# Optimization experiments

Measured on AMD Instinct MI355X. Metric: run time of the kernel, lower is better.

## Reference

```python
import jax, jax.numpy as jnp
import numpy as np

OUT_H, OUT_W = 512, 512


def setup_inputs() -> dict:
    key = jax.random.key(0)
    k1, k2 = jax.random.split(key)
    U = jax.random.normal(k1, (8, 512, 512, 16), dtype=jnp.float32)
    # coarse deformation field (x/y offsets in normalized [-1,1] coords)
    flow = jax.random.normal(k2, (8, 64, 64, 2), dtype=jnp.float32) * 0.1
    return {"U": U, "flow": flow}


def _grid_sample_bilinear(U, x, y):
    """Faithful port of _interpolate: x, y in [-1,1] normalized coords, shape [B,oh,ow].
    Note the original maps (x+1)*W/2 (not (W-1)/2) and computes weights from the
    CLIPPED corner coordinates — we replicate that exactly."""
    B, H, W, C = U.shape
    x = (x + 1.0) * (W / 2.0)
    y = (y + 1.0) * (H / 2.0)
    x0 = jnp.floor(x).astype(jnp.int32)
    x1 = x0 + 1
    y0 = jnp.floor(y).astype(jnp.int32)
    y1 = y0 + 1
    x0 = jnp.clip(x0, 0, W - 1)
    x1 = jnp.clip(x1, 0, W - 1)
    y0 = jnp.clip(y0, 0, H - 1)
    y1 = jnp.clip(y1, 0, H - 1)
    b = jnp.arange(B, dtype=jnp.int32)[:, None, None]  # broadcast over oh, ow
    Ia = U[b, y0, x0]  # [B,oh,ow,C]
    Ib = U[b, y1, x0]
    Ic = U[b, y0, x1]
    Id = U[b, y1, x1]
    x0f = x0.astype(jnp.float32); x1f = x1.astype(jnp.float32)
    y0f = y0.astype(jnp.float32); y1f = y1.astype(jnp.float32)
    wa = ((x1f - x) * (y1f - y))[..., None]
    wb = ((x1f - x) * (y - y0f))[..., None]
    wc = ((x - x0f) * (y1f - y))[..., None]
    wd = ((x - x0f) * (y - y0f))[..., None]
    return wa * Ia + wb * Ib + wc * Ic + wd * Id


def reference(U, flow):
    B, H, W, C = U.shape
    # bicubic upsample of the coarse deformation field to output resolution
    V = jax.image.resize(flow, (B, OUT_H, OUT_W, 2), method="cubic")  # [B,oh,ow,2]
    # identity sampling grid in [-1,1]
    xs = jnp.linspace(-1.0, 1.0, OUT_W, dtype=jnp.float32)
    ys = jnp.linspace(-1.0, 1.0, OUT_H, dtype=jnp.float32)
    Xg, Yg = jnp.meshgrid(xs, ys)  # [oh,ow]
    x_s = V[..., 0] + Xg  # [B,oh,ow]
    y_s = V[..., 1] + Yg
    return _grid_sample_bilinear(U, x_s, y_s)  # [B,oh,ow,C]
```

## Files before the change

### kernel.cpp

```cpp
#include <hip/hip_runtime.h>


#define N_B    8
#define IN_HW  512
#define N_C    16
#define F_HW   64
#define OUTHW  512
#define TILE   16

typedef float fvec4 __attribute__((ext_vector_type(4)));

__device__ __forceinline__ float keys_w(float x) {
    if (x >= 2.0f) return 0.0f;
    if (x >= 1.0f) return ((-0.5f * x + 2.5f) * x - 4.0f) * x + 2.0f;
    return ((1.5f * x - 2.5f) * x) * x + 1.0f;
}

__device__ __forceinline__ int cubic_taps(int i, float w[4]) {
    float sf = (i + 0.5f) * 0.125f - 0.5f;
    int jf = (int)floorf(sf);
    float sum = 0.0f;
#pragma unroll
    for (int t = 0; t < 4; ++t) {
        int j = jf - 1 + t;
        float wt = 0.0f;
        if (j >= 0 && j < F_HW) wt = keys_w(fabsf(sf - (float)j));
        w[t] = wt;
        sum += wt;
    }
    float inv = 1.0f / sum;
#pragma unroll
    for (int t = 0; t < 4; ++t) w[t] *= inv;
    return jf - 1;
}

__global__ __launch_bounds__(256) void sdt_kernel(const float* __restrict__ U,
                                                  const float* __restrict__ flow,
                                                  float* __restrict__ out) {
    __shared__ float2 coords[TILE * TILE];

    const int tid = threadIdx.x;
    const int b  = blockIdx.x & 7;
    const int t  = blockIdx.x >> 3;
    const int tx = t & 31;
    const int ty = t >> 5;

    {
        const int px = tid & (TILE - 1);
        const int py = tid >> 4;
        const int ox = tx * TILE + px;
        const int oy = ty * TILE + py;

        float wx[4], wy[4];
        const int jx0 = cubic_taps(ox, wx);
        const int jy0 = cubic_taps(oy, wy);

        float vx = 0.0f, vy = 0.0f;
        const float* fb = flow + (size_t)b * (F_HW * F_HW * 2);
#pragma unroll
        for (int s = 0; s < 4; ++s) {
            const int jy = min(max(jy0 + s, 0), F_HW - 1);
            const float wyt = wy[s];
            const float* frow = fb + jy * (F_HW * 2);
#pragma unroll
            for (int r = 0; r < 4; ++r) {
                const int jx = min(max(jx0 + r, 0), F_HW - 1);
                const float w = wyt * wx[r];
                const float2 f2 = *(const float2*)(frow + jx * 2);
                vx = fmaf(w, f2.x, vx);
                vy = fmaf(w, f2.y, vy);
            }
        }
        const float xg = -1.0f + (2.0f / 511.0f) * (float)ox;
        const float yg = -1.0f + (2.0f / 511.0f) * (float)oy;
        coords[tid] = make_float2((vx + xg + 1.0f) * (IN_HW / 2.0f),
                                  (vy + yg + 1.0f) * (IN_HW / 2.0f));
    }
    __syncthreads();

    const int chg  = tid & 3;
    const int slot = tid >> 2;
#pragma unroll
    for (int it = 0; it < 4; ++it) {
        const int q  = it * 64 + slot;
        const float2 c = coords[q];
        const float x = c.x, y = c.y;

        const float fx0 = floorf(x);
        const float fy0 = floorf(y);
        const int x0 = min(max((int)fx0, 0), IN_HW - 1);
        const int x1 = min(max((int)fx0 + 1, 0), IN_HW - 1);
        const int y0 = min(max((int)fy0, 0), IN_HW - 1);
        const int y1 = min(max((int)fy0 + 1, 0), IN_HW - 1);
        const float x0f = (float)x0, x1f = (float)x1, y0f = (float)y0, y1f = (float)y1;
        const float wa = (x1f - x) * (y1f - y);
        const float wb = (x1f - x) * (y - y0f);
        const float wc = (x - x0f) * (y1f - y);
        const float wd = (x - x0f) * (y - y0f);

        const fvec4 a  = *((const fvec4*)(U + (((size_t)b * IN_HW + y0) * IN_HW + x0) * N_C) + chg);
        const fvec4 bb = *((const fvec4*)(U + (((size_t)b * IN_HW + y1) * IN_HW + x0) * N_C) + chg);
        const fvec4 cc = *((const fvec4*)(U + (((size_t)b * IN_HW + y0) * IN_HW + x1) * N_C) + chg);
        const fvec4 dd = *((const fvec4*)(U + (((size_t)b * IN_HW + y1) * IN_HW + x1) * N_C) + chg);
        fvec4 r = wa * a + wb * bb + wc * cc + wd * dd;

        const int ox = tx * TILE + (q & (TILE - 1));
        const int oy = ty * TILE + (q >> 4);
        fvec4* O = (fvec4*)(out + (((size_t)b * OUTHW + oy) * OUTHW + ox) * N_C) + chg;
        __builtin_nontemporal_store(r, O);
    }
}

extern "C" void kernel_launch(void* const* d_in, const int* in_sizes, int n_in,
                              void* d_out, int out_size, void* d_ws, size_t ws_size,
                              hipStream_t stream) {
    const float* U    = (const float*)d_in[0];
    const float* flow = (const float*)d_in[1];
    float* out        = (float*)d_out;
    const int n_blocks = N_B * (OUTHW / TILE) * (OUTHW / TILE);
    sdt_kernel<<<dim3(n_blocks), dim3(256), 0, stream>>>(U, flow, out);
}
```

Measured before the change: 51.54 us.

## Separate bicubic flow upsampling into shared-memory row and column passes

Replaces the per-pixel 4x4 bicubic flow interpolation with a separable scheme. Per-tile tap weights go to shared memory, then a horizontal pass produces 6 filtered rows, then a vertical pass gives each pixel's flow. This cuts the redundant 16 global flow loads and the weight computation in every thread, at the cost of two extra block barriers. It also adds a launch-bounds occupancy hint and hoists the batch base pointer for U.

Result: faster. 46.83 us (-9.2%).

```diff
diff --git a/kernel.cpp b/kernel.cpp
--- a/kernel.cpp
+++ b/kernel.cpp
@@ -34,9 +34,14 @@
     return jf - 1;
 }
 
-__global__ __launch_bounds__(256) void sdt_kernel(const float* __restrict__ U,
-                                                  const float* __restrict__ flow,
-                                                  float* __restrict__ out) {
+__global__ __launch_bounds__(256, 4) void sdt_kernel(const float* __restrict__ U,
+                                                     const float* __restrict__ flow,
+                                                     float* __restrict__ out) {
+    __shared__ float  wx4[TILE][4];
+    __shared__ int    jx0s[TILE];
+    __shared__ float  wy4[TILE][4];
+    __shared__ int    djy[TILE];
+    __shared__ float2 Hs[6][TILE + 1];
     __shared__ float2 coords[TILE * TILE];
 
     const int tid = threadIdx.x;
@@ -44,33 +49,58 @@
     const int t  = blockIdx.x >> 3;
     const int tx = t & 31;
     const int ty = t >> 5;
+    const int jxB = 2 * tx - 2;
+    const int jyB = 2 * ty - 2;
+
+    const float* fb = flow + (size_t)b * (F_HW * F_HW * 2);
+
+    if (tid < 16) {
+        float w[4];
+        const int base = cubic_taps(tx * TILE + tid, w);
+        wx4[tid][0] = w[0]; wx4[tid][1] = w[1]; wx4[tid][2] = w[2]; wx4[tid][3] = w[3];
+        jx0s[tid] = base;
+    } else if (tid < 32) {
+        const int py = tid - 16;
+        float w[4];
+        const int base = cubic_taps(ty * TILE + py, w);
+        wy4[py][0] = w[0]; wy4[py][1] = w[1]; wy4[py][2] = w[2]; wy4[py][3] = w[3];
+        djy[py] = base - jyB;
+    }
+    __syncthreads();
+
+    if (tid < 96) {
+        const int jrow = tid >> 4;
+        const int col  = tid & 15;
+        const int row  = min(max(jyB + jrow, 0), F_HW - 1);
+        const float2* frow = (const float2*)fb + row * F_HW;
+        const int base = jx0s[col];
+        float hx = 0.0f, hy = 0.0f;
+#pragma unroll
+        for (int r = 0; r < 4; ++r) {
+            const int jx = min(max(base + r, 0), F_HW - 1);
+            const float w = wx4[col][r];
+            const float2 f2 = frow[jx];
+            hx = fmaf(w, f2.x, hx);
+            hy = fmaf(w, f2.y, hy);
+        }
+        Hs[jrow][col] = make_float2(hx, hy);
+    }
+    __syncthreads();
 
     {
-        const int px = tid & (TILE - 1);
+        const int px = tid & 15;
         const int py = tid >> 4;
+        const int dj = djy[py];
+        float vx = 0.0f, vy = 0.0f;
+#pragma unroll
+        for (int s = 0; s < 4; ++s) {
+            const float w = wy4[py][s];
+            const float2 h = Hs[dj + s][px];
+            vx = fmaf(w, h.x, vx);
+            vy = fmaf(w, h.y, vy);
+        }
         const int ox = tx * TILE + px;
         const int oy = ty * TILE + py;
-
-        float wx[4], wy[4];
-        const int jx0 = cubic_taps(ox, wx);
-        const int jy0 = cubic_taps(oy, wy);
-
-        float vx = 0.0f, vy = 0.0f;
-        const float* fb = flow + (size_t)b * (F_HW * F_HW * 2);
-#pragma unroll
-        for (int s = 0; s < 4; ++s) {
-            const int jy = min(max(jy0 + s, 0), F_HW - 1);
-            const float wyt = wy[s];
-            const float* frow = fb + jy * (F_HW * 2);
-#pragma unroll
-            for (int r = 0; r < 4; ++r) {
-                const int jx = min(max(jx0 + r, 0), F_HW - 1);
-                const float w = wyt * wx[r];
-                const float2 f2 = *(const float2*)(frow + jx * 2);
-                vx = fmaf(w, f2.x, vx);
-                vy = fmaf(w, f2.y, vy);
-            }
-        }
         const float xg = -1.0f + (2.0f / 511.0f) * (float)ox;
         const float yg = -1.0f + (2.0f / 511.0f) * (float)oy;
         coords[tid] = make_float2((vx + xg + 1.0f) * (IN_HW / 2.0f),
@@ -80,6 +110,7 @@
 
     const int chg  = tid & 3;
     const int slot = tid >> 2;
+    const float* Ub = U + (size_t)b * (IN_HW * IN_HW * N_C);
 #pragma unroll
     for (int it = 0; it < 4; ++it) {
         const int q  = it * 64 + slot;
@@ -98,13 +129,13 @@
         const float wc = (x - x0f) * (y1f - y);
         const float wd = (x - x0f) * (y - y0f);
 
-        const fvec4 a  = *((const fvec4*)(U + (((size_t)b * IN_HW + y0) * IN_HW + x0) * N_C) + chg);
-        const fvec4 bb = *((const fvec4*)(U + (((size_t)b * IN_HW + y1) * IN_HW + x0) * N_C) + chg);
-        const fvec4 cc = *((const fvec4*)(U + (((size_t)b * IN_HW + y0) * IN_HW + x1) * N_C) + chg);
-        const fvec4 dd = *((const fvec4*)(U + (((size_t)b * IN_HW + y1) * IN_HW + x1) * N_C) + chg);
-        fvec4 r = wa * a + wb * bb + wc * cc + wd * dd;
+        const fvec4 a  = *((const fvec4*)(Ub + ((size_t)y0 * IN_HW + x0) * N_C) + chg);
+        const fvec4 bb = *((const fvec4*)(Ub + ((size_t)y1 * IN_HW + x0) * N_C) + chg);
+        const fvec4 cc = *((const fvec4*)(Ub + ((size_t)y0 * IN_HW + x1) * N_C) + chg);
+        const fvec4 dd = *((const fvec4*)(Ub + ((size_t)y1 * IN_HW + x1) * N_C) + chg);
+        const fvec4 r = wa * a + wb * bb + wc * cc + wd * dd;
 
-        const int ox = tx * TILE + (q & (TILE - 1));
+        const int ox = tx * TILE + (q & 15);
         const int oy = ty * TILE + (q >> 4);
         fvec4* O = (fvec4*)(out + (((size_t)b * OUTHW + oy) * OUTHW + ox) * N_C) + chg;
         __builtin_nontemporal_store(r, O);
```
